# Kernel tuning notes

Hardware: AMD Instinct MI355X
Metric: run time of the kernel (lower is better)

Reference implementation:

```python
import jax, jax.numpy as jnp
import numpy as np

FP4_AMAX = 6.0
FP8_AMAX = 448.0
E2M1_LUT = jnp.array([0.0, 0.5, 1.0, 1.5, 2.0, 3.0, 4.0, 6.0], dtype=jnp.float32)
# (threshold, code) pairs; applied in order, alternating <= and < comparisons
THRESHOLDS = [(5.0, 6), (3.5, 5), (2.5, 4), (1.75, 3), (1.25, 2), (0.75, 1), (0.25, 0)]


def _fp4_code(a):
    # a: abs-values, float32. Round-to-e2m1 magnitude code per the torch threshold table.
    code = jnp.full(a.shape, 7, dtype=jnp.int32)
    for i, (m, c) in enumerate(THRESHOLDS):
        mask = (a <= m) if i % 2 == 0 else (a < m)
        code = jnp.where(mask, c, code)
    return code


def simulate_nvfp4_quantize(w):
    # w: (out, in), in % 16 == 0. Returns fake-quantized weight, same shape/dtype.
    out_f, in_f = w.shape
    wb = w.reshape(out_f, in_f // 16, 16).astype(jnp.float32)
    gs = (FP4_AMAX * FP8_AMAX) / jnp.max(jnp.abs(wb))          # global fp32 scale
    s_decb = jnp.max(jnp.abs(wb), axis=-1) / FP4_AMAX           # per-16-block decode scale
    xs = jnp.clip(s_decb * gs, -FP8_AMAX, FP8_AMAX).astype(jnp.float8_e4m3fn)  # fp8 block scales
    xs_f = xs.astype(jnp.float32)
    s_encb = gs / jnp.clip(xs_f, 1e-12, None)                   # encode scale per block
    x_scaled = wb * s_encb[..., None]
    sign = jnp.where(jnp.signbit(x_scaled), -1.0, 1.0)
    mag = E2M1_LUT[_fp4_code(jnp.abs(x_scaled))]
    wq = sign * mag * (xs_f / gs)[..., None]                    # dequantize
    return wq.reshape(out_f, in_f).astype(w.dtype)


def setup_inputs() -> dict:
    key = jax.random.key(0)
    k1, k2, k3 = jax.random.split(key, 3)
    B, S, IN, OUT = 4, 2048, 4096, 4096
    x = jax.random.normal(k1, (B, S, IN), dtype=jnp.float32)
    weight = jax.random.normal(k2, (OUT, IN), dtype=jnp.float32) * 0.02
    bias = jax.random.normal(k3, (OUT,), dtype=jnp.float32) * 0.01
    return {"x": x, "weight": weight, "bias": bias}


def reference(x, weight, bias):
    # STE quantization: forward uses fake-quant weight
    weight_q = simulate_nvfp4_quantize(weight)
    # F.linear: x @ W^T + b
    return jnp.einsum("bsi,oi->bso", x, weight_q) + bias
```

## Files before the change

kernel.cpp:

```cpp
#include <hip/hip_runtime.h>
#include <hip/hip_bf16.h>
#include <stdint.h>

typedef __bf16 bf16_t;
typedef __bf16 bf16x8 __attribute__((ext_vector_type(8)));
typedef float  f32x4  __attribute__((ext_vector_type(4)));

#define BM 256
#define BN 128
#define BK 32
#define NTHREADS 512

__global__ void k_absmax(const float* __restrict__ w, unsigned int* __restrict__ out_bits, int n4) {
    int i = blockIdx.x * blockDim.x + threadIdx.x;
    int stride = gridDim.x * blockDim.x;
    const float4* w4 = (const float4*)w;
    float m = 0.0f;
    for (; i < n4; i += stride) {
        float4 v = w4[i];
        m = fmaxf(m, fmaxf(fmaxf(fabsf(v.x), fabsf(v.y)), fmaxf(fabsf(v.z), fabsf(v.w))));
    }
    #pragma unroll
    for (int off = 32; off; off >>= 1)
        m = fmaxf(m, __shfl_xor(m, off));
    if ((threadIdx.x & 63) == 0)
        atomicMax(out_bits, __float_as_uint(m));
}

__device__ __forceinline__ float e4m3_rne(float v) {
    if (v < 0.015625f) {
        return rintf(v * 512.0f) * (1.0f / 512.0f);
    }
    unsigned int u = __float_as_uint(v);
    unsigned int keep = u >> 20;
    unsigned int r = u & 0xFFFFFu;
    if (r > 0x80000u || (r == 0x80000u && (keep & 1u))) keep++;
    return __uint_as_float(keep << 20);
}

__global__ void k_quantize(const float* __restrict__ w, bf16_t* __restrict__ wq,
                           const unsigned int* __restrict__ maxbits, int nblk) {
    int t = blockIdx.x * blockDim.x + threadIdx.x;
    if (t >= nblk) return;
    float gmax = __uint_as_float(*maxbits);
    float gs = 2688.0f / gmax;
    const float4* w4 = (const float4*)w + (size_t)t * 4;
    float4 v0 = w4[0], v1 = w4[1], v2 = w4[2], v3 = w4[3];
    float vv[16];
    vv[0]=v0.x; vv[1]=v0.y; vv[2]=v0.z; vv[3]=v0.w;
    vv[4]=v1.x; vv[5]=v1.y; vv[6]=v1.z; vv[7]=v1.w;
    vv[8]=v2.x; vv[9]=v2.y; vv[10]=v2.z; vv[11]=v2.w;
    vv[12]=v3.x; vv[13]=v3.y; vv[14]=v3.z; vv[15]=v3.w;
    float bmax = 0.0f;
    #pragma unroll
    for (int j = 0; j < 16; ++j) bmax = fmaxf(bmax, fabsf(vv[j]));
    float s_decb = bmax / 6.0f;
    float xs_in  = fminf(s_decb * gs, 448.0f);
    float xs_f   = e4m3_rne(xs_in);
    float s_encb = gs / fmaxf(xs_f, 1e-12f);
    float dscale = xs_f / gs;
    bf16x8 o0, o1;
    #pragma unroll
    for (int j = 0; j < 16; ++j) {
        float xsc = vv[j] * s_encb;
        float a = fabsf(xsc);
        float mag = (a <= 0.25f) ? 0.0f
                  : (a <  0.75f) ? 0.5f
                  : (a <= 1.25f) ? 1.0f
                  : (a <  1.75f) ? 1.5f
                  : (a <= 2.5f ) ? 2.0f
                  : (a <  3.5f ) ? 3.0f
                  : (a <= 5.0f ) ? 4.0f : 6.0f;
        float sgn = __builtin_copysignf(1.0f, xsc);
        float val = (sgn * mag) * dscale;
        if (j < 8) o0[j] = (bf16_t)val; else o1[j - 8] = (bf16_t)val;
    }
    *(bf16x8*)(wq + (size_t)t * 16)     = o0;
    *(bf16x8*)(wq + (size_t)t * 16 + 8) = o1;
}

__global__ void k_cvt_x(const float* __restrict__ x, bf16_t* __restrict__ xb, long n8) {
    long i = blockIdx.x * (long)blockDim.x + threadIdx.x;
    long stride = (long)gridDim.x * blockDim.x;
    const float4* x4 = (const float4*)x;
    for (; i < n8; i += stride) {
        float4 a = x4[2 * i], b = x4[2 * i + 1];
        bf16x8 o;
        o[0] = (bf16_t)a.x; o[1] = (bf16_t)a.y; o[2] = (bf16_t)a.z; o[3] = (bf16_t)a.w;
        o[4] = (bf16_t)b.x; o[5] = (bf16_t)b.y; o[6] = (bf16_t)b.z; o[7] = (bf16_t)b.w;
        *(bf16x8*)(xb + i * 8) = o;
    }
}

__device__ __forceinline__ void BARRIER() {
    asm volatile("" ::: "memory");
    __builtin_amdgcn_s_barrier();
    asm volatile("" ::: "memory");
}

__device__ __forceinline__ void gload16(const bf16_t* g, bf16_t* l) {
    __builtin_amdgcn_global_load_lds(
        (const __attribute__((address_space(1))) unsigned int*)g,
        (__attribute__((address_space(3))) unsigned int*)l,
        16, 0, 0);
}

__device__ __forceinline__ int swzg(int row, int g) {
    return (row << 2) + (g ^ (row & 3) ^ ((row >> 2) & 3));
}

__global__ __launch_bounds__(NTHREADS, 4) void k_gemm(
        const bf16_t* __restrict__ A,
        const bf16_t* __restrict__ Bt,
        const float*  __restrict__ bias,
        float* __restrict__ C, int M, int N, int K) {
    __shared__ __align__(16) bf16_t sA[3][BM * BK];
    __shared__ __align__(16) bf16_t sB[3][BN * BK];

    int bid = blockIdx.x;
    int cpx = gridDim.x >> 3;
    int swz = (bid & 7) * cpx + (bid >> 3);
    int nbn = N / BN;
    int m0 = (swz / nbn) * BM, n0 = (swz % nbn) * BN;

    int tid  = threadIdx.x;
    int lane = tid & 63;
    int w    = tid >> 6;
    int wr   = w >> 1, wc = w & 1;
    int fr   = lane & 15;
    int gq   = lane >> 4;

    int gaof[2], laof[2], gbof, lbof;
    #pragma unroll
    for (int r = 0; r < 2; ++r) {
        int pf  = r * 512 + tid;
        int row = pf >> 2;
        int lg  = (pf & 3) ^ (row & 3) ^ ((row >> 2) & 3);
        gaof[r] = row * K + lg * 8;
        laof[r] = pf * 8;
    }
    {
        int pf  = tid;
        int row = pf >> 2;
        int lg  = (pf & 3) ^ (row & 3) ^ ((row >> 2) & 3);
        gbof = row * K + lg * 8;
        lbof = pf * 8;
    }
    const bf16_t* Ab = A  + (size_t)m0 * K;
    const bf16_t* Bb = Bt + (size_t)n0 * K;

#define STAGE(DA, DB, KK) do {                              \
        gload16(Ab + gaof[0] + (KK), (DA) + laof[0]);       \
        gload16(Ab + gaof[1] + (KK), (DA) + laof[1]);       \
        gload16(Bb + gbof    + (KK), (DB) + lbof);          \
    } while (0)

    int aof[4], bof[4];
    #pragma unroll
    for (int i = 0; i < 4; ++i) aof[i] = swzg(wr * 64 + i * 16 + fr, gq) * 8;
    #pragma unroll
    for (int j = 0; j < 4; ++j) bof[j] = swzg(wc * 64 + j * 16 + fr, gq) * 8;

    f32x4 acc[4][4] = {};

    bf16_t *cA0 = sA[0], *cA1 = sA[1], *cA2 = sA[2];
    bf16_t *cB0 = sB[0], *cB1 = sB[1], *cB2 = sB[2];

    const int NT = K / BK;

    STAGE(cA0, cB0, 0);
    STAGE(cA1, cB1, BK);
    asm volatile("s_waitcnt vmcnt(3)" ::: "memory");
    BARRIER();

    for (int t = 0; t < NT; ++t) {
        bf16x8 af[4], bf[4];
        #pragma unroll
        for (int i = 0; i < 4; ++i) af[i] = *(const bf16x8*)(cA0 + aof[i]);
        #pragma unroll
        for (int j = 0; j < 4; ++j) bf[j] = *(const bf16x8*)(cB0 + bof[j]);

        if (t + 2 < NT)
            STAGE(cA2, cB2, (t + 2) * BK);

        __builtin_amdgcn_s_setprio(1);
        #pragma unroll
        for (int i = 0; i < 4; ++i)
            #pragma unroll
            for (int j = 0; j < 4; ++j)
                acc[i][j] = __builtin_amdgcn_mfma_f32_16x16x32_bf16(af[i], bf[j], acc[i][j], 0, 0, 0);
        __builtin_amdgcn_s_setprio(0);

        if (t + 2 < NT) {
            asm volatile("s_waitcnt vmcnt(3)" ::: "memory");
        } else {
            asm volatile("s_waitcnt vmcnt(0)" ::: "memory");
        }
        BARRIER();

        bf16_t* tp;
        tp = cA0; cA0 = cA1; cA1 = cA2; cA2 = tp;
        tp = cB0; cB0 = cB1; cB1 = cB2; cB2 = tp;
    }

    int crow = (lane >> 4) * 4;
    int ccol = lane & 15;
    float bv[4];
    #pragma unroll
    for (int j = 0; j < 4; ++j) bv[j] = bias[n0 + wc * 64 + j * 16 + ccol];
    #pragma unroll
    for (int i = 0; i < 4; ++i) {
        size_t mrow = (size_t)(m0 + wr * 64 + i * 16 + crow);
        #pragma unroll
        for (int j = 0; j < 4; ++j) {
            float* cp = C + mrow * N + (n0 + wc * 64 + j * 16 + ccol);
            #pragma unroll
            for (int r = 0; r < 4; ++r)
                cp[(size_t)r * N] = acc[i][j][r] + bv[j];
        }
    }
#undef STAGE
}

extern "C" void kernel_launch(void* const* d_in, const int* in_sizes, int n_in,
                              void* d_out, int out_size, void* d_ws, size_t ws_size,
                              hipStream_t stream) {
    const float* x    = (const float*)d_in[0];
    const float* wgt  = (const float*)d_in[1];
    const float* bias = (const float*)d_in[2];
    float* out = (float*)d_out;

    const int N = in_sizes[2];
    const int K = in_sizes[1] / N;
    const int M = in_sizes[0] / K;

    unsigned int* maxbits = (unsigned int*)d_ws;
    bf16_t* wq = (bf16_t*)((char*)d_ws + 256);
    bf16_t* xb = (bf16_t*)((char*)d_ws + 256 + (size_t)N * K * sizeof(bf16_t));

    hipMemsetAsync(d_ws, 0, 256, stream);
    k_absmax<<<512, 256, 0, stream>>>(wgt, maxbits, N * K / 4);
    int nblk = N * K / 16;
    k_quantize<<<(nblk + 255) / 256, 256, 0, stream>>>(wgt, wq, maxbits, nblk);
    long n8 = (long)M * K / 8;
    k_cvt_x<<<2048, 256, 0, stream>>>(x, xb, n8);
    dim3 grid((M / BM) * (N / BN));
    k_gemm<<<grid, NTHREADS, 0, stream>>>(xb, wq, bias, out, M, N, K);
}
```

Before: 366.7 us.

## Enlarge GEMM tile to 256x256 and switch to 32x32x16 MFMA

Widens the block tile from 256x128 to 256x256 and remaps the 8 waves into a 2x4 grid, each computing a 128x64 sub-tile with 32x32x16 bf16 MFMA instructions instead of 16x16x32. A fragments are loaded from LDS one step ahead of the MFMAs that consume them, which overlaps LDS reads with matrix math. The aim is more arithmetic per byte loaded from global memory and LDS, with fewer, larger MFMAs. In exchange, accumulator registers and LDS per block both grow, so launch bounds drop to 2 blocks per CU and occupancy is lower.

```diff
diff --git a/kernel.cpp b/kernel.cpp
--- a/kernel.cpp
+++ b/kernel.cpp
@@ -4,10 +4,10 @@
 
 typedef __bf16 bf16_t;
 typedef __bf16 bf16x8 __attribute__((ext_vector_type(8)));
-typedef float  f32x4  __attribute__((ext_vector_type(4)));
+typedef float  f32x16 __attribute__((ext_vector_type(16)));
 
 #define BM 256
-#define BN 128
+#define BN 256
 #define BK 32
 #define NTHREADS 512
 
@@ -109,7 +109,7 @@
     return (row << 2) + (g ^ (row & 3) ^ ((row >> 2) & 3));
 }
 
-__global__ __launch_bounds__(NTHREADS, 4) void k_gemm(
+__global__ __launch_bounds__(NTHREADS, 2) void k_gemm(
         const bf16_t* __restrict__ A,
         const bf16_t* __restrict__ Bt,
         const float*  __restrict__ bias,
@@ -126,42 +126,37 @@
     int tid  = threadIdx.x;
     int lane = tid & 63;
     int w    = tid >> 6;
-    int wr   = w >> 1, wc = w & 1;
-    int fr   = lane & 15;
-    int gq   = lane >> 4;
-
-    int gaof[2], laof[2], gbof, lbof;
+    int wr   = w >> 2, wc = w & 3;
+    int fr   = lane & 31;
+    int hi   = lane >> 5;
+
+    int gof[2], lof[2];
     #pragma unroll
     for (int r = 0; r < 2; ++r) {
         int pf  = r * 512 + tid;
         int row = pf >> 2;
         int lg  = (pf & 3) ^ (row & 3) ^ ((row >> 2) & 3);
-        gaof[r] = row * K + lg * 8;
-        laof[r] = pf * 8;
-    }
-    {
-        int pf  = tid;
-        int row = pf >> 2;
-        int lg  = (pf & 3) ^ (row & 3) ^ ((row >> 2) & 3);
-        gbof = row * K + lg * 8;
-        lbof = pf * 8;
+        gof[r] = row * K + lg * 8;
+        lof[r] = pf * 8;
     }
     const bf16_t* Ab = A  + (size_t)m0 * K;
     const bf16_t* Bb = Bt + (size_t)n0 * K;
 
 #define STAGE(DA, DB, KK) do {                              \
-        gload16(Ab + gaof[0] + (KK), (DA) + laof[0]);       \
-        gload16(Ab + gaof[1] + (KK), (DA) + laof[1]);       \
-        gload16(Bb + gbof    + (KK), (DB) + lbof);          \
+        gload16(Ab + gof[0] + (KK), (DA) + lof[0]);         \
+        gload16(Ab + gof[1] + (KK), (DA) + lof[1]);         \
+        gload16(Bb + gof[0] + (KK), (DB) + lof[0]);         \
+        gload16(Bb + gof[1] + (KK), (DB) + lof[1]);         \
     } while (0)
 
-    int aof[4], bof[4];
-    #pragma unroll
-    for (int i = 0; i < 4; ++i) aof[i] = swzg(wr * 64 + i * 16 + fr, gq) * 8;
-    #pragma unroll
-    for (int j = 0; j < 4; ++j) bof[j] = swzg(wc * 64 + j * 16 + fr, gq) * 8;
-
-    f32x4 acc[4][4] = {};
+    int aof[2], bof[2];
+    #pragma unroll
+    for (int kk = 0; kk < 2; ++kk) {
+        aof[kk] = swzg(wr * 128 + fr, (kk << 1) + hi) * 8;
+        bof[kk] = swzg(wc * 64  + fr, (kk << 1) + hi) * 8;
+    }
+
+    f32x16 acc[4][2] = {};
 
     bf16_t *cA0 = sA[0], *cA1 = sA[1], *cA2 = sA[2];
     bf16_t *cB0 = sB[0], *cB1 = sB[1], *cB2 = sB[2];
@@ -170,29 +165,38 @@
 
     STAGE(cA0, cB0, 0);
     STAGE(cA1, cB1, BK);
-    asm volatile("s_waitcnt vmcnt(3)" ::: "memory");
+    asm volatile("s_waitcnt vmcnt(4)" ::: "memory");
     BARRIER();
 
     for (int t = 0; t < NT; ++t) {
-        bf16x8 af[4], bf[4];
-        #pragma unroll
-        for (int i = 0; i < 4; ++i) af[i] = *(const bf16x8*)(cA0 + aof[i]);
-        #pragma unroll
-        for (int j = 0; j < 4; ++j) bf[j] = *(const bf16x8*)(cB0 + bof[j]);
-
         if (t + 2 < NT)
             STAGE(cA2, cB2, (t + 2) * BK);
 
+        bf16x8 bf00 = *(const bf16x8*)(cB0 + bof[0]);
+        bf16x8 bf01 = *(const bf16x8*)(cB0 + bof[1]);
+        bf16x8 bf10 = *(const bf16x8*)(cB0 + 1024 + bof[0]);
+        bf16x8 bf11 = *(const bf16x8*)(cB0 + 1024 + bof[1]);
+        bf16x8 a0 = *(const bf16x8*)(cA0 + aof[0]);
+        bf16x8 a1 = *(const bf16x8*)(cA0 + aof[1]);
+
         __builtin_amdgcn_s_setprio(1);
         #pragma unroll
-        for (int i = 0; i < 4; ++i)
-            #pragma unroll
-            for (int j = 0; j < 4; ++j)
-                acc[i][j] = __builtin_amdgcn_mfma_f32_16x16x32_bf16(af[i], bf[j], acc[i][j], 0, 0, 0);
+        for (int mi = 0; mi < 4; ++mi) {
+            bf16x8 n0f, n1f;
+            if (mi < 3) {
+                n0f = *(const bf16x8*)(cA0 + (mi + 1) * 1024 + aof[0]);
+                n1f = *(const bf16x8*)(cA0 + (mi + 1) * 1024 + aof[1]);
+            }
+            acc[mi][0] = __builtin_amdgcn_mfma_f32_32x32x16_bf16(a0, bf00, acc[mi][0], 0, 0, 0);
+            acc[mi][0] = __builtin_amdgcn_mfma_f32_32x32x16_bf16(a1, bf01, acc[mi][0], 0, 0, 0);
+            acc[mi][1] = __builtin_amdgcn_mfma_f32_32x32x16_bf16(a0, bf10, acc[mi][1], 0, 0, 0);
+            acc[mi][1] = __builtin_amdgcn_mfma_f32_32x32x16_bf16(a1, bf11, acc[mi][1], 0, 0, 0);
+            if (mi < 3) { a0 = n0f; a1 = n1f; }
+        }
         __builtin_amdgcn_s_setprio(0);
 
         if (t + 2 < NT) {
-            asm volatile("s_waitcnt vmcnt(3)" ::: "memory");
+            asm volatile("s_waitcnt vmcnt(4)" ::: "memory");
         } else {
             asm volatile("s_waitcnt vmcnt(0)" ::: "memory");
         }
@@ -203,20 +207,20 @@
         tp = cB0; cB0 = cB1; cB1 = cB2; cB2 = tp;
     }
 
-    int crow = (lane >> 4) * 4;
-    int ccol = lane & 15;
-    float bv[4];
-    #pragma unroll
-    for (int j = 0; j < 4; ++j) bv[j] = bias[n0 + wc * 64 + j * 16 + ccol];
-    #pragma unroll
-    for (int i = 0; i < 4; ++i) {
-        size_t mrow = (size_t)(m0 + wr * 64 + i * 16 + crow);
+    int ccol = lane & 31;
+    float bv[2];
+    #pragma unroll
+    for (int j = 0; j < 2; ++j) bv[j] = bias[n0 + wc * 64 + j * 32 + ccol];
+    #pragma unroll
+    for (int mi = 0; mi < 4; ++mi) {
         #pragma unroll
-        for (int j = 0; j < 4; ++j) {
-            float* cp = C + mrow * N + (n0 + wc * 64 + j * 16 + ccol);
+        for (int j = 0; j < 2; ++j) {
+            size_t cb = (size_t)(m0 + wr * 128 + mi * 32) * N + (n0 + wc * 64 + j * 32 + ccol);
             #pragma unroll
-            for (int r = 0; r < 4; ++r)
-                cp[(size_t)r * N] = acc[i][j][r] + bv[j];
+            for (int reg = 0; reg < 16; ++reg) {
+                int row = (reg & 3) + 8 * (reg >> 2) + 4 * hi;
+                C[cb + (size_t)row * N] = acc[mi][j][reg] + bv[j];
+            }
         }
     }
 #undef STAGE
```

Measured after the change: 400.0 us. 9.1% more time.
